# Kernel optimization log

Hardware: AMD Instinct MI355X
Metric: run time of the kernel (lower is better)

## Reference

```python
import jax, jax.numpy as jnp
import numpy as np

HID = 128
N_LAYERS = 6


def _init_linear(key, fan_in, fan_out, scale=None):
    kw, kb = jax.random.split(key)
    s = scale if scale is not None else (1.0 / np.sqrt(fan_in))
    W = jax.random.uniform(kw, (fan_in, fan_out), jnp.float32, -s, s)
    b = jnp.zeros((fan_out,), jnp.float32)
    return W, b


def setup_inputs() -> dict:
    key = jax.random.key(0)
    ks = jax.random.split(key, 16)
    N, E, EC = 50000, 600000, 100000
    x = jax.random.normal(ks[0], (N, 9), jnp.float32)
    edge_index = jax.random.randint(ks[1], (2, E), 0, N, jnp.int64)
    edge_attr = jax.random.normal(ks[2], (E, 11), jnp.float32)
    connectivity = jax.random.randint(ks[3], (EC, 2), 0, N, jnp.int64)
    bc_disp = (jax.random.uniform(ks[4], (N, 1)) < 0.1).astype(jnp.float32)
    prop_I22 = jax.random.uniform(ks[5], (EC,), jnp.float32)

    enc_W1, enc_b1 = _init_linear(ks[6], 9, HID)
    enc_W2, enc_b2 = _init_linear(ks[7], HID, HID)
    # per-layer GN params stacked along axis 0
    msg_in = 2 * HID + 11
    mk = jax.random.split(ks[8], N_LAYERS)
    uk = jax.random.split(ks[9], N_LAYERS)
    mk2 = jax.random.split(ks[10], N_LAYERS)
    msg_W1 = jnp.stack([_init_linear(mk[i], msg_in, HID)[0] for i in range(N_LAYERS)])
    msg_b1 = jnp.zeros((N_LAYERS, HID), jnp.float32)
    msg_W2 = jnp.stack([_init_linear(mk2[i], HID, HID)[0] for i in range(N_LAYERS)])
    msg_b2 = jnp.zeros((N_LAYERS, HID), jnp.float32)
    upd_W = jnp.stack([_init_linear(uk[i], 2 * HID, HID)[0] for i in range(N_LAYERS)])
    upd_b = jnp.zeros((N_LAYERS, HID), jnp.float32)

    ef_W1, ef_b1 = _init_linear(ks[11], 1 + 2 * HID, 64)
    ef_W2, ef_b2 = _init_linear(ks[12], 64, 64)
    ef_W3, ef_b3 = _init_linear(ks[13], 64, 3, scale=0.1 * np.sqrt(6.0 / (64 + 3)))

    return dict(x=x, edge_index=edge_index, edge_attr=edge_attr,
                connectivity=connectivity, bc_disp=bc_disp, prop_I22=prop_I22,
                n_quad_pts=5,
                enc_W1=enc_W1, enc_b1=enc_b1, enc_W2=enc_W2, enc_b2=enc_b2,
                msg_W1=msg_W1, msg_b1=msg_b1, msg_W2=msg_W2, msg_b2=msg_b2,
                upd_W=upd_W, upd_b=upd_b,
                ef_W1=ef_W1, ef_b1=ef_b1, ef_W2=ef_W2, ef_b2=ef_b2,
                ef_W3=ef_W3, ef_b3=ef_b3)


def reference(x, edge_index, edge_attr, connectivity, bc_disp, prop_I22, n_quad_pts,
              enc_W1, enc_b1, enc_W2, enc_b2,
              msg_W1, msg_b1, msg_W2, msg_b2, upd_W, upd_b,
              ef_W1, ef_b1, ef_W2, ef_b2, ef_W3, ef_b3):
    N = x.shape[0]
    silu = jax.nn.silu
    # encoder MLP
    h = silu(x @ enc_W1 + enc_b1)
    h = silu(h @ enc_W2 + enc_b2)
    src, dst = edge_index[0], edge_index[1]
    for l in range(N_LAYERS):
        m_in = jnp.concatenate([h[src], h[dst], edge_attr], axis=-1)  # (E, 2H+11)
        m = silu(m_in @ msg_W1[l] + msg_b1[l]) @ msg_W2[l] + msg_b2[l]
        agg = jax.ops.segment_sum(m, dst, num_segments=N)  # scatter-add
        h = jnp.concatenate([h, agg], axis=-1) @ upd_W[l] + upd_b[l] + h  # residual update
        h = silu(h)
    # continuous edge field evaluation
    n1, n2 = connectivity[:, 0], connectivity[:, 1]
    EC = connectivity.shape[0]
    xi_1d = jnp.linspace(0.0, 1.0, n_quad_pts, dtype=jnp.float32)
    xi = jnp.broadcast_to(xi_1d[None, :, None], (EC, n_quad_pts, 1))
    h_i = jnp.broadcast_to(h[n1][:, None, :], (EC, n_quad_pts, HID))
    h_j = jnp.broadcast_to(h[n2][:, None, :], (EC, n_quad_pts, HID))
    inp = jnp.concatenate([xi, h_i, h_j], axis=-1)  # (EC, n_pts, 1+2H)
    f = silu(inp @ ef_W1 + ef_b1)
    f = silu(f @ ef_W2 + ef_b2)
    fields = f @ ef_W3 + ef_b3  # (EC, n_pts, 3)
    # hard BCs
    bc_mask = bc_disp[:, 0]
    bc_i, bc_j = bc_mask[n1], bc_mask[n2]
    xi_vals = xi[..., 0]
    mask_i = 1.0 - bc_i[:, None] * (1.0 - xi_vals)
    mask_j = 1.0 - bc_j[:, None] * xi_vals
    fields = fields * (mask_i * mask_j)[..., None]
    return h, xi, fields, prop_I22
```

## Files before the change

### kernel.cpp

```cpp
#include <hip/hip_runtime.h>
#include <hip/hip_bf16.h>

#define HID 128
#define EA_DIM 11
#define MSG_IN (2 * HID + EA_DIM)
#define TILE_E 128
#define KCAP 272
#define KB (KCAP * 2)
#define MSG_LDS 139264

typedef __attribute__((ext_vector_type(8))) short short8;
typedef __attribute__((ext_vector_type(16))) float f32x16;
typedef __attribute__((ext_vector_type(4))) float float4v;

__device__ __forceinline__ float siluf(float x) { return x / (1.f + __expf(-x)); }
__device__ __forceinline__ short f2bf(float f) {
    __hip_bfloat16 h = __float2bfloat16(f);
    return *reinterpret_cast<short*>(&h);
}
__device__ __forceinline__ int crow(int r, int khalf) { return (r & 3) + 8 * (r >> 2) + 4 * khalf; }

__global__ __launch_bounds__(128) void encoder_kernel(
    const float* __restrict__ x, const float* __restrict__ W1, const float* __restrict__ b1,
    const float* __restrict__ W2, const float* __restrict__ b2,
    float* __restrict__ h, short* __restrict__ hb)
{
    int i = blockIdx.x, j = threadIdx.x;
    __shared__ float xs[9];
    __shared__ float t1[HID];
    if (j < 9) xs[j] = x[(size_t)i * 9 + j];
    __syncthreads();
    float acc = b1[j];
    #pragma unroll
    for (int k = 0; k < 9; ++k) acc = fmaf(xs[k], W1[k * HID + j], acc);
    t1[j] = siluf(acc);
    __syncthreads();
    float acc2 = b2[j];
    #pragma unroll 8
    for (int k = 0; k < HID; ++k) acc2 = fmaf(t1[k], W2[k * HID + j], acc2);
    float v = siluf(acc2);
    h[(size_t)i * HID + j] = v;
    if (hb) hb[(size_t)i * HID + j] = f2bf(v);
}

__global__ void convert_w_kernel(
    const float* __restrict__ msgW1, const float* __restrict__ msgW2,
    const float* __restrict__ updW,
    const float* __restrict__ efW1, const float* __restrict__ efW2, const float* __restrict__ efW3,
    short* __restrict__ w1t, short* __restrict__ w2t, short* __restrict__ updwt,
    short* __restrict__ efw1t, short* __restrict__ efw2t, short* __restrict__ efw3t, int nl)
{
    int gid = blockIdx.x * blockDim.x + threadIdx.x;
    int n1 = nl * 128 * (KCAP / 8);
    int n2 = nl * 128 * (HID / 8);
    int n3 = nl * 128 * 32;
    int n4 = 64 * 32, n5 = 64 * 8, n6 = 32 * 8;
    short8 v;
    if (gid < n1) {
        int c = gid % (KCAP / 8);
        int rem = gid / (KCAP / 8);
        int n = rem % 128, lay = rem / 128;
        #pragma unroll
        for (int j = 0; j < 8; ++j) {
            int k = c * 8 + j;
            v[j] = (k < MSG_IN) ? f2bf(msgW1[(size_t)lay * MSG_IN * HID + (size_t)k * HID + n]) : (short)0;
        }
        *(short8*)(w1t + ((size_t)lay * 128 + n) * KCAP + c * 8) = v;
    } else if (gid < n1 + n2) {
        int g = gid - n1;
        int c = g % (HID / 8);
        int rem = g / (HID / 8);
        int n = rem % 128, lay = rem / 128;
        #pragma unroll
        for (int j = 0; j < 8; ++j)
            v[j] = f2bf(msgW2[(size_t)lay * HID * HID + (size_t)(c * 8 + j) * HID + n]);
        *(short8*)(w2t + ((size_t)lay * 128 + n) * HID + c * 8) = v;
    } else if (gid < n1 + n2 + n3) {
        int g = gid - n1 - n2;
        int c = g & 31;
        int rem = g >> 5;
        int n = rem & 127, lay = rem >> 7;
        #pragma unroll
        for (int j = 0; j < 8; ++j)
            v[j] = f2bf(updW[(size_t)lay * 256 * 128 + (size_t)(c * 8 + j) * 128 + n]);
        *(short8*)(updwt + ((size_t)lay * 128 + n) * 256 + c * 8) = v;
    } else if (gid < n1 + n2 + n3 + n4) {
        int g = gid - n1 - n2 - n3;
        int c = g & 31, n = g >> 5;
        #pragma unroll
        for (int j = 0; j < 8; ++j)
            v[j] = f2bf(efW1[(size_t)(c * 8 + j + 1) * 64 + n]);
        *(short8*)(efw1t + (size_t)n * 256 + c * 8) = v;
    } else if (gid < n1 + n2 + n3 + n4 + n5) {
        int g = gid - n1 - n2 - n3 - n4;
        int c = g & 7, n = g >> 3;
        #pragma unroll
        for (int j = 0; j < 8; ++j)
            v[j] = f2bf(efW2[(size_t)(c * 8 + j) * 64 + n]);
        *(short8*)(efw2t + (size_t)n * 64 + c * 8) = v;
    } else if (gid < n1 + n2 + n3 + n4 + n5 + n6) {
        int g = gid - n1 - n2 - n3 - n4 - n5;
        int c = g & 7, n = g >> 3;
        #pragma unroll
        for (int j = 0; j < 8; ++j)
            v[j] = (n < 3) ? f2bf(efW3[(size_t)(c * 8 + j) * 3 + n]) : (short)0;
        *(short8*)(efw3t + (size_t)n * 64 + c * 8) = v;
    }
}

__global__ void hist_kernel(const int* __restrict__ ei, int* __restrict__ cnt, int E)
{
    for (int e = blockIdx.x * blockDim.x + threadIdx.x; e < E; e += gridDim.x * blockDim.x)
        atomicAdd(&cnt[ei[(size_t)E + e]], 1);
}
__global__ __launch_bounds__(256) void scanA_kernel(const int* __restrict__ cnt, int* __restrict__ btot, int N)
{
    __shared__ int s[256];
    int i = blockIdx.x * 256 + threadIdx.x;
    s[threadIdx.x] = (i < N) ? cnt[i] : 0;
    __syncthreads();
    for (int o = 128; o > 0; o >>= 1) {
        if (threadIdx.x < o) s[threadIdx.x] += s[threadIdx.x + o];
        __syncthreads();
    }
    if (threadIdx.x == 0) btot[blockIdx.x] = s[0];
}
__global__ __launch_bounds__(1024) void scanB_kernel(int* __restrict__ btot, int nb)
{
    __shared__ int s[1024];
    int t = threadIdx.x;
    int v = (t < nb) ? btot[t] : 0;
    s[t] = v;
    __syncthreads();
    for (int o = 1; o < 1024; o <<= 1) {
        int tv = 0;
        if (t >= o) tv = s[t - o];
        __syncthreads();
        s[t] += tv;
        __syncthreads();
    }
    if (t < nb) btot[t] = s[t] - v;
}
__global__ __launch_bounds__(256) void scanC_kernel(const int* __restrict__ cnt, const int* __restrict__ btot,
                                                    int* __restrict__ cur, int N)
{
    __shared__ int s[256];
    int i = blockIdx.x * 256 + threadIdx.x;
    int t = threadIdx.x;
    int v = (i < N) ? cnt[i] : 0;
    s[t] = v;
    __syncthreads();
    for (int o = 1; o < 256; o <<= 1) {
        int tv = 0;
        if (t >= o) tv = s[t - o];
        __syncthreads();
        s[t] += tv;
        __syncthreads();
    }
    if (i < N) cur[i] = btot[blockIdx.x] + s[t] - v;
}
__global__ void scatter_kernel(const int* __restrict__ ei, int* __restrict__ cur,
                               int* __restrict__ eord, int E)
{
    for (int e = blockIdx.x * blockDim.x + threadIdx.x; e < E; e += gridDim.x * blockDim.x) {
        int d = ei[(size_t)E + e];
        int p = atomicAdd(&cur[d], 1);
        eord[p] = e;
    }
}
__global__ void reorder_kernel(const int* __restrict__ ei, const float* __restrict__ ea,
                               const int* __restrict__ eord,
                               int* __restrict__ srcs_s, int* __restrict__ dsts_s,
                               short* __restrict__ ea_s, int E)
{
    for (int p = blockIdx.x * blockDim.x + threadIdx.x; p < E; p += gridDim.x * blockDim.x) {
        int es = eord[p];
        srcs_s[p] = ei[es];
        dsts_s[p] = ei[(size_t)E + es];
        short tv[16];
        #pragma unroll
        for (int j = 0; j < 16; ++j) tv[j] = 0;
        #pragma unroll
        for (int j = 0; j < EA_DIM; ++j) tv[j] = f2bf(ea[(size_t)es * EA_DIM + j]);
        short8 v0, v1;
        #pragma unroll
        for (int j = 0; j < 8; ++j) { v0[j] = tv[j]; v1[j] = tv[8 + j]; }
        *(short8*)(ea_s + (size_t)p * 16) = v0;
        *(short8*)(ea_s + (size_t)p * 16 + 8) = v1;
    }
}

__global__ __launch_bounds__(512, 1) void msg_mfma_kernel(
    const float* __restrict__ h, const short* __restrict__ hb,
    const int* __restrict__ ei, const float* __restrict__ ea,
    const int* __restrict__ srcs_s, const int* __restrict__ dsts_s, const short* __restrict__ ea_s,
    const short* __restrict__ w1t, const float* __restrict__ b1,
    const short* __restrict__ w2t, const float* __restrict__ b2,
    float* __restrict__ agg, int E, int ntiles)
{
    extern __shared__ char smem[];
    char* sA = smem + 69632;
    __shared__ int dsts[TILE_E];

    int tid = threadIdx.x, ln = tid & 63, wave = tid >> 6;
    int mh = wave & 1, nq4 = wave >> 1;
    int l31 = ln & 31, khalf = ln >> 5;

    {
        int row = tid & 127, grp = tid >> 7;
        for (int c = grp; c < 34; c += 4) {
            short8 v = *(const short8*)(w1t + (size_t)row * KCAP + c * 8);
            *(short8*)(smem + ((row * KB + c * 16) ^ ((row & 7) << 4))) = v;
        }
    }

    int col = nq4 * 32 + l31;
    float b1v = b1[col], b2v = b2[col];
    short8 zer;
    #pragma unroll
    for (int j = 0; j < 8; ++j) zer[j] = 0;
    int ar0 = mh * 64 + l31;
    const short8* w2r = (const short8*)(w2t + (size_t)col * HID);

    bool sorted = (ea_s != nullptr) && (hb != nullptr);

    int pr = tid >> 2, pq = tid & 3;
    int pf_idx = 0; bool pf_valid = false;
    short8 pf_h[8];
    short8 pf_e0 = zer, pf_e1 = zer;

    if (sorted) {
        long ep = (long)blockIdx.x * TILE_E + pr;
        pf_valid = ep < E;
        pf_idx = pf_valid ? ((pq < 2) ? srcs_s[ep] : dsts_s[ep]) : 0;
        const short8* hr8 = (const short8*)(hb + (size_t)pf_idx * HID + (pq & 1) * 64);
        #pragma unroll
        for (int c = 0; c < 8; ++c) pf_h[c] = hr8[c];
        if (pq == 3 && pf_valid) {
            pf_e0 = *(const short8*)(ea_s + (size_t)ep * 16);
            pf_e1 = *(const short8*)(ea_s + (size_t)ep * 16 + 8);
        }
    }

    #pragma unroll 1
    for (int tile = blockIdx.x; tile < ntiles; tile += gridDim.x) {
        __syncthreads();

        if (sorted) {
            int dbase = (pq >> 1) * 256 + (pq & 1) * 128;
            #pragma unroll
            for (int c = 0; c < 8; ++c) {
                short8 v = pf_valid ? pf_h[c] : zer;
                *(short8*)(sA + ((pr * KB + dbase + c * 16) ^ ((pr & 7) << 4))) = v;
            }
            if (pq == 2) dsts[pr] = pf_valid ? pf_idx : -1;
            if (pq == 3) {
                *(short8*)(sA + ((pr * KB + 512) ^ ((pr & 7) << 4))) = pf_valid ? pf_e0 : zer;
                *(short8*)(sA + ((pr * KB + 528) ^ ((pr & 7) << 4))) = pf_valid ? pf_e1 : zer;
            }
        } else {
            int r = pr, q = pq;
            long ep = (long)tile * TILE_E + r;
            bool valid = ep < E;
            int idx = 0;
            if (valid) idx = (q < 2) ? ei[ep] : ei[(size_t)E + ep];
            int half = q & 1;
            int dbase = (q >> 1) * 256 + half * 128;
            if (hb) {
                const short8* hr8 = (const short8*)(hb + (size_t)idx * HID + half * 64);
                #pragma unroll
                for (int c = 0; c < 8; ++c) {
                    short8 v = valid ? hr8[c] : zer;
                    *(short8*)(sA + ((r * KB + dbase + c * 16) ^ ((r & 7) << 4))) = v;
                }
            } else {
                const float* hr = h + (size_t)idx * HID + half * 64;
                #pragma unroll
                for (int c = 0; c < 8; ++c) {
                    short8 v = zer;
                    if (valid) {
                        float4v f0 = *(const float4v*)(hr + c * 8);
                        float4v f1 = *(const float4v*)(hr + c * 8 + 4);
                        #pragma unroll
                        for (int j = 0; j < 4; ++j) { v[j] = f2bf(f0[j]); v[4 + j] = f2bf(f1[j]); }
                    }
                    *(short8*)(sA + ((r * KB + dbase + c * 16) ^ ((r & 7) << 4))) = v;
                }
            }
            if (q == 2) dsts[r] = valid ? idx : -1;
            if (q == 3) {
                short8 v0 = zer, v1 = zer;
                if (valid) {
                    short tv[16];
                    #pragma unroll
                    for (int j = 0; j < 16; ++j) tv[j] = 0;
                    #pragma unroll
                    for (int j = 0; j < EA_DIM; ++j) tv[j] = f2bf(ea[(size_t)ep * EA_DIM + j]);
                    #pragma unroll
                    for (int j = 0; j < 8; ++j) { v0[j] = tv[j]; v1[j] = tv[8 + j]; }
                }
                *(short8*)(sA + ((r * KB + 512) ^ ((r & 7) << 4))) = v0;
                *(short8*)(sA + ((r * KB + 528) ^ ((r & 7) << 4))) = v1;
            }
        }
        __syncthreads();

        if (sorted) {
            long ep = (long)(tile + gridDim.x) * TILE_E + pr;
            pf_valid = ep < E;
            pf_idx = pf_valid ? ((pq < 2) ? srcs_s[ep] : dsts_s[ep]) : 0;
            const short8* hr8 = (const short8*)(hb + (size_t)pf_idx * HID + (pq & 1) * 64);
            #pragma unroll
            for (int c = 0; c < 8; ++c) pf_h[c] = hr8[c];
            if (pq == 3 && pf_valid) {
                pf_e0 = *(const short8*)(ea_s + (size_t)ep * 16);
                pf_e1 = *(const short8*)(ea_s + (size_t)ep * 16 + 8);
            }
        }

        f32x16 acc1[2] = {};
        for (int kk = 0; kk < 17; ++kk) {
            int kb = kk * 32 + khalf * 16;
            short8 a0 = *(short8*)(sA + ((ar0 * KB + kb) ^ ((ar0 & 7) << 4)));
            short8 a1 = *(short8*)(sA + (((ar0 + 32) * KB + kb) ^ (((ar0 + 32) & 7) << 4)));
            short8 w  = *(short8*)(smem + ((col * KB + kb) ^ ((col & 7) << 4)));
            acc1[0] = __builtin_amdgcn_mfma_f32_32x32x16_bf16(a0, w, acc1[0], 0, 0, 0);
            acc1[1] = __builtin_amdgcn_mfma_f32_32x32x16_bf16(a1, w, acc1[1], 0, 0, 0);
        }
        __syncthreads();

        #pragma unroll
        for (int mi = 0; mi < 2; ++mi)
            #pragma unroll
            for (int r = 0; r < 16; ++r) {
                float s = siluf(acc1[mi][r] + b1v);
                int row = mh * 64 + mi * 32 + crow(r, khalf);
                *(short*)(sA + ((row * 256 + col * 2) ^ ((row & 7) << 4))) = f2bf(s);
            }
        __syncthreads();

        f32x16 acc2[2];
        #pragma unroll
        for (int mi = 0; mi < 2; ++mi)
            #pragma unroll
            for (int r = 0; r < 16; ++r) acc2[mi][r] = b2v;
        for (int kk = 0; kk < 8; ++kk) {
            int kb = kk * 32 + khalf * 16;
            short8 a0 = *(short8*)(sA + ((ar0 * 256 + kb) ^ ((ar0 & 7) << 4)));
            short8 a1 = *(short8*)(sA + (((ar0 + 32) * 256 + kb) ^ (((ar0 + 32) & 7) << 4)));
            short8 w  = w2r[kk * 2 + khalf];
            acc2[0] = __builtin_amdgcn_mfma_f32_32x32x16_bf16(a0, w, acc2[0], 0, 0, 0);
            acc2[1] = __builtin_amdgcn_mfma_f32_32x32x16_bf16(a1, w, acc2[1], 0, 0, 0);
        }

        if (sorted) {
            __syncthreads();
            #pragma unroll
            for (int mi = 0; mi < 2; ++mi)
                #pragma unroll
                for (int r = 0; r < 16; ++r) {
                    int row = mh * 64 + mi * 32 + crow(r, khalf);
                    *(float*)(sA + row * 512 + col * 4) = acc2[mi][r];
                }
            __syncthreads();
            {
                int c2 = tid & 63, g = tid >> 6;
                float s0 = 0.f, s1 = 0.f;
                int dprev = -1;
                #pragma unroll 1
                for (int rr = 0; rr < 16; ++rr) {
                    int row = g * 16 + rr;
                    int d = dsts[row];
                    float2 v = *(float2*)(sA + row * 512 + c2 * 8);
                    if (d != dprev) {
                        if (dprev >= 0) {
                            atomicAdd(agg + (size_t)dprev * HID + c2 * 2,     s0);
                            atomicAdd(agg + (size_t)dprev * HID + c2 * 2 + 1, s1);
                        }
                        s0 = 0.f; s1 = 0.f; dprev = d;
                    }
                    if (d >= 0) { s0 += v.x; s1 += v.y; }
                }
                if (dprev >= 0) {
                    atomicAdd(agg + (size_t)dprev * HID + c2 * 2,     s0);
                    atomicAdd(agg + (size_t)dprev * HID + c2 * 2 + 1, s1);
                }
            }
        } else {
            #pragma unroll
            for (int mi = 0; mi < 2; ++mi)
                #pragma unroll
                for (int r = 0; r < 16; ++r) {
                    int row = mh * 64 + mi * 32 + crow(r, khalf);
                    int d = dsts[row];
                    if (d >= 0) atomicAdd(agg + (size_t)d * HID + col, acc2[mi][r]);
                }
        }
    }
}

__global__ __launch_bounds__(256) void upd_mfma_kernel(
    float* __restrict__ h, short* __restrict__ hb, const float* __restrict__ agg,
    const short* __restrict__ updwt, const float* __restrict__ b, int N, int ntiles)
{
    __shared__ char sA[64 * 512];
    int tid = threadIdx.x, ln = tid & 63, wave = tid >> 6;
    int mhalf = wave & 1, nhalf = wave >> 1, l31 = ln & 31, khalf = ln >> 5;
    float bv[2];
    #pragma unroll
    for (int ni = 0; ni < 2; ++ni) bv[ni] = b[nhalf * 64 + ni * 32 + l31];
    short8 zer;
    #pragma unroll
    for (int j = 0; j < 8; ++j) zer[j] = 0;

    #pragma unroll 1
    for (int tile = blockIdx.x; tile < ntiles; tile += gridDim.x) {
        __syncthreads();
        {
            int r = tid >> 2, q = tid & 3;
            int node = tile * 64 + r;
            bool valid = node < N;
            if (q < 2) {
                if (hb) {
                    const short8* hr8 = (const short8*)(hb + (size_t)node * HID + (q & 1) * 64);
                    #pragma unroll
                    for (int c = 0; c < 8; ++c) {
                        short8 v = valid ? hr8[c] : zer;
                        *(short8*)(sA + ((r * 512 + (q & 1) * 128 + c * 16) ^ ((r & 7) << 4))) = v;
                    }
                } else {
                    const float* hr = h + (size_t)node * HID + (q & 1) * 64;
                    #pragma unroll
                    for (int c = 0; c < 8; ++c) {
                        short8 v = zer;
                        if (valid) {
                            float4v f0 = *(const float4v*)(hr + c * 8);
                            float4v f1 = *(const float4v*)(hr + c * 8 + 4);
                            #pragma unroll
                            for (int j = 0; j < 4; ++j) { v[j] = f2bf(f0[j]); v[4 + j] = f2bf(f1[j]); }
                        }
                        *(short8*)(sA + ((r * 512 + (q & 1) * 128 + c * 16) ^ ((r & 7) << 4))) = v;
                    }
                }
            } else {
                const float* ar = agg + (size_t)node * HID + (q & 1) * 64;
                #pragma unroll
                for (int c = 0; c < 8; ++c) {
                    short8 v = zer;
                    if (valid) {
                        float4v f0 = *(const float4v*)(ar + c * 8);
                        float4v f1 = *(const float4v*)(ar + c * 8 + 4);
                        #pragma unroll
                        for (int j = 0; j < 4; ++j) { v[j] = f2bf(f0[j]); v[4 + j] = f2bf(f1[j]); }
                    }
                    *(short8*)(sA + ((r * 512 + 256 + (q & 1) * 128 + c * 16) ^ ((r & 7) << 4))) = v;
                }
            }
        }
        __syncthreads();
        f32x16 acc[2] = {};
        int arow = mhalf * 32 + l31;
        const short* bp0 = updwt + (size_t)(nhalf * 64 + l31) * 256 + khalf * 8;
        const short* bp1 = updwt + (size_t)(nhalf * 64 + 32 + l31) * 256 + khalf * 8;
        for (int kk = 0; kk < 16; ++kk) {
            short8 a  = *(short8*)(sA + ((arow * 512 + kk * 32 + khalf * 16) ^ ((arow & 7) << 4)));
            short8 w0 = *(const short8*)(bp0 + kk * 16);
            short8 w1 = *(const short8*)(bp1 + kk * 16);
            acc[0] = __builtin_amdgcn_mfma_f32_32x32x16_bf16(a, w0, acc[0], 0, 0, 0);
            acc[1] = __builtin_amdgcn_mfma_f32_32x32x16_bf16(a, w1, acc[1], 0, 0, 0);
        }
        #pragma unroll
        for (int ni = 0; ni < 2; ++ni) {
            int col = nhalf * 64 + ni * 32 + l31;
            #pragma unroll
            for (int r = 0; r < 16; ++r) {
                int node = tile * 64 + mhalf * 32 + crow(r, khalf);
                if (node < N) {
                    float val = siluf(acc[ni][r] + bv[ni] + h[(size_t)node * HID + col]);
                    h[(size_t)node * HID + col] = val;
                    if (hb) hb[(size_t)node * HID + col] = f2bf(val);
                }
            }
        }
    }
}

__global__ __launch_bounds__(256) void fields_mfma_kernel(
    const float* __restrict__ h, const short* __restrict__ hb,
    const int* __restrict__ conn, const float* __restrict__ bc,
    const float* __restrict__ efW1, const float* __restrict__ efb1,
    const float* __restrict__ efb2, const float* __restrict__ efb3,
    const short* __restrict__ efw1t, const short* __restrict__ efw2t, const short* __restrict__ efw3t,
    float* __restrict__ f_out, int EC, int nq, int ntiles)
{
    __shared__ char sA1[64 * 512];
    __shared__ char sA2[64 * 128];
    __shared__ char sF2[64 * 128];
    __shared__ float bcis[64], bcjs[64];
    int tid = threadIdx.x, ln = tid & 63, wave = tid >> 6;
    int mhalf = wave & 1, nhalf = wave >> 1, l31 = ln & 31, khalf = ln >> 5;
    int col = nhalf * 32 + l31;
    float w1x = efW1[col];
    float b1v = efb1[col], b2v = efb2[col];
    float b3v = (l31 < 3) ? efb3[l31] : 0.f;
    float inv = (nq > 1) ? 1.f / (float)(nq - 1) : 0.f;
    short8 zer;
    #pragma unroll
    for (int j = 0; j < 8; ++j) zer[j] = 0;

    #pragma unroll 1
    for (int tile = blockIdx.x; tile < ntiles; tile += gridDim.x) {
        __syncthreads();
        {
            int r = tid >> 2, q = tid & 3;
            long p = (long)tile * 64 + r;
            bool valid = p < EC;
            int node = 0;
            if (valid) node = conn[p * 2 + (q >> 1)];
            if (q == 0) {
                bcis[r] = valid ? bc[conn[p * 2]] : 0.f;
                bcjs[r] = valid ? bc[conn[p * 2 + 1]] : 0.f;
            }
            int cbyte = (q >> 1) * 256 + (q & 1) * 128;
            if (hb) {
                const short8* hr8 = (const short8*)(hb + (size_t)node * HID + (q & 1) * 64);
                #pragma unroll
                for (int c = 0; c < 8; ++c) {
                    short8 v = valid ? hr8[c] : zer;
                    *(short8*)(sA1 + ((r * 512 + cbyte + c * 16) ^ ((r & 7) << 4))) = v;
                }
            } else {
                const float* hr = h + (size_t)node * HID + (q & 1) * 64;
                #pragma unroll
                for (int c = 0; c < 8; ++c) {
                    short8 v = zer;
                    if (valid) {
                        float4v f0 = *(const float4v*)(hr + c * 8);
                        float4v f1 = *(const float4v*)(hr + c * 8 + 4);
                        #pragma unroll
                        for (int j = 0; j < 4; ++j) { v[j] = f2bf(f0[j]); v[4 + j] = f2bf(f1[j]); }
                    }
                    *(short8*)(sA1 + ((r * 512 + cbyte + c * 16) ^ ((r & 7) << 4))) = v;
                }
            }
        }
        __syncthreads();
        f32x16 hp = {};
        int arow = mhalf * 32 + l31;
        for (int kk = 0; kk < 16; ++kk) {
            short8 a = *(short8*)(sA1 + ((arow * 512 + kk * 32 + khalf * 16) ^ ((arow & 7) << 4)));
            short8 b = *(const short8*)(efw1t + (size_t)col * 256 + kk * 16 + khalf * 8);
            hp = __builtin_amdgcn_mfma_f32_32x32x16_bf16(a, b, hp, 0, 0, 0);
        }
        #pragma unroll
        for (int r = 0; r < 16; ++r) hp[r] += b1v;

        for (int q = 0; q < nq; ++q) {
            float xi = (float)q * inv;
            #pragma unroll
            for (int r = 0; r < 16; ++r) {
                float f1 = siluf(fmaf(xi, w1x, hp[r]));
                int row = mhalf * 32 + crow(r, khalf);
                *(short*)(sA2 + ((row * 128 + col * 2) ^ ((row & 7) << 4))) = f2bf(f1);
            }
            __syncthreads();
            f32x16 f2a = {};
            for (int kk = 0; kk < 4; ++kk) {
                short8 a = *(short8*)(sA2 + ((arow * 128 + kk * 32 + khalf * 16) ^ ((l31 & 7) << 4)));
                short8 b = *(const short8*)(efw2t + (size_t)col * 64 + kk * 16 + khalf * 8);
                f2a = __builtin_amdgcn_mfma_f32_32x32x16_bf16(a, b, f2a, 0, 0, 0);
            }
            #pragma unroll
            for (int r = 0; r < 16; ++r) {
                float f2 = siluf(f2a[r] + b2v);
                int row = mhalf * 32 + crow(r, khalf);
                *(short*)(sF2 + ((row * 128 + col * 2) ^ ((row & 7) << 4))) = f2bf(f2);
            }
            __syncthreads();
            f32x16 oa = {};
            for (int kk = 0; kk < 4; ++kk) {
                short8 a = *(short8*)(sF2 + ((arow * 128 + kk * 32 + khalf * 16) ^ ((l31 & 7) << 4)));
                short8 b = *(const short8*)(efw3t + (size_t)l31 * 64 + kk * 16 + khalf * 8);
                oa = __builtin_amdgcn_mfma_f32_32x32x16_bf16(a, b, oa, 0, 0, 0);
            }
            if (nhalf == 0 && l31 < 3) {
                #pragma unroll
                for (int r = 0; r < 16; ++r) {
                    int row = mhalf * 32 + crow(r, khalf);
                    long p = (long)tile * 64 + row;
                    if (p < EC) {
                        float mask = (1.f - bcis[row] * (1.f - xi)) * (1.f - bcjs[row] * xi);
                        f_out[((size_t)p * nq + q) * 3 + l31] = (oa[r] + b3v) * mask;
                    }
                }
            }
        }
    }
}

__global__ void aux_kernel(const float* __restrict__ prop, float* __restrict__ out_p,
                           float* __restrict__ out_xi, int EC, int nq, float inv)
{
    int i = blockIdx.x * blockDim.x + threadIdx.x;
    if (i < EC) out_p[i] = prop[i];
    if (i < EC * nq) out_xi[i] = (float)(i % nq) * inv;
}

extern "C" void kernel_launch(void* const* d_in, const int* in_sizes, int n_in,
                              void* d_out, int out_size, void* d_ws, size_t ws_size,
                              hipStream_t stream) {
    const float* x     = (const float*)d_in[0];
    const int*   ei    = (const int*)d_in[1];
    const float* ea    = (const float*)d_in[2];
    const int*   conn  = (const int*)d_in[3];
    const float* bc    = (const float*)d_in[4];
    const float* prop  = (const float*)d_in[5];
    const float* encW1 = (const float*)d_in[7];
    const float* encb1 = (const float*)d_in[8];
    const float* encW2 = (const float*)d_in[9];
    const float* encb2 = (const float*)d_in[10];
    const float* msgW1 = (const float*)d_in[11];
    const float* msgb1 = (const float*)d_in[12];
    const float* msgW2 = (const float*)d_in[13];
    const float* msgb2 = (const float*)d_in[14];
    const float* updW  = (const float*)d_in[15];
    const float* updb  = (const float*)d_in[16];
    const float* efW1  = (const float*)d_in[17];
    const float* efb1  = (const float*)d_in[18];
    const float* efW2  = (const float*)d_in[19];
    const float* efb2  = (const float*)d_in[20];
    const float* efW3  = (const float*)d_in[21];
    const float* efb3  = (const float*)d_in[22];

    int N  = in_sizes[0] / 9;
    int E  = in_sizes[1] / 2;
    int EC = in_sizes[5];
    int nl = in_sizes[11] / (MSG_IN * HID);
    int nq = (int)(((long long)out_size - (long long)N * HID - EC) / (4LL * EC));

    float* out    = (float*)d_out;
    float* h      = out;
    float* out_xi = out + (size_t)N * HID;
    float* out_f  = out_xi + (size_t)EC * nq;
    float* out_p  = out_f + (size_t)EC * nq * 3;

    size_t w1t_e = (size_t)nl * 128 * KCAP;
    size_t w2t_e = (size_t)nl * 128 * HID;
    size_t updwt_e = (size_t)nl * 128 * 256;
    size_t efw1t_e = 64 * 256, efw2t_e = 64 * 64, efw3t_e = 32 * 64;
    short* w1t   = (short*)d_ws;
    short* w2t   = w1t + w1t_e;
    short* updwt = w2t + w2t_e;
    short* efw1t = updwt + updwt_e;
    short* efw2t = efw1t + efw1t_e;
    short* efw3t = efw2t + efw2t_e;
    size_t wbytes = (w1t_e + w2t_e + updwt_e + efw1t_e + efw2t_e + efw3t_e) * 2;
    wbytes = (wbytes + 255) & ~(size_t)255;
    size_t hb_bytes  = (size_t)N * HID * 2;
    size_t agg_bytes = (size_t)N * HID * 4;
    size_t sort_bytes = ((size_t)2 * N + 1024 + (size_t)3 * E) * 4 + (size_t)E * 32;

    short* hb = nullptr;
    float* agg;
    int *icnt = nullptr, *icur = nullptr, *btot = nullptr, *eord = nullptr;
    int *srcs_s = nullptr, *dsts_s = nullptr;
    short* ea_s = nullptr;
    if (ws_size >= wbytes + hb_bytes + agg_bytes + sort_bytes) {
        char* p = (char*)d_ws + wbytes;
        hb = (short*)p;      p += hb_bytes;
        agg = (float*)p;     p += agg_bytes;
        icnt = (int*)p;      p += (size_t)N * 4;
        icur = (int*)p;      p += (size_t)N * 4;
        btot = (int*)p;      p += 1024 * 4;
        eord = (int*)p;      p += (size_t)E * 4;
        srcs_s = (int*)p;    p += (size_t)E * 4;
        dsts_s = (int*)p;    p += (size_t)E * 4;
        ea_s = (short*)p;
    } else if (ws_size >= wbytes + hb_bytes + agg_bytes) {
        hb  = (short*)((char*)d_ws + wbytes);
        agg = (float*)((char*)d_ws + wbytes + hb_bytes);
    } else {
        agg = (float*)((char*)d_ws + wbytes);
    }

    hipFuncSetAttribute((const void*)msg_mfma_kernel,
                        hipFuncAttributeMaxDynamicSharedMemorySize, MSG_LDS);

    encoder_kernel<<<N, 128, 0, stream>>>(x, encW1, encb1, encW2, encb2, h, hb);

    {
        int chunks = nl * 128 * (KCAP / 8) + nl * 128 * (HID / 8) + nl * 128 * 32
                   + 64 * 32 + 64 * 8 + 32 * 8;
        convert_w_kernel<<<(chunks + 255) / 256, 256, 0, stream>>>(
            msgW1, msgW2, updW, efW1, efW2, efW3,
            w1t, w2t, updwt, efw1t, efw2t, efw3t, nl);
    }

    if (ea_s) {
        int nb = (N + 255) / 256;
        hipMemsetAsync(icnt, 0, (size_t)N * 4, stream);
        hist_kernel<<<512, 256, 0, stream>>>(ei, icnt, E);
        scanA_kernel<<<nb, 256, 0, stream>>>(icnt, btot, N);
        scanB_kernel<<<1, 1024, 0, stream>>>(btot, nb);
        scanC_kernel<<<nb, 256, 0, stream>>>(icnt, btot, icur, N);
        scatter_kernel<<<512, 256, 0, stream>>>(ei, icur, eord, E);
        reorder_kernel<<<512, 256, 0, stream>>>(ei, ea, eord, srcs_s, dsts_s, ea_s, E);
    }

    int ntiles = (E + TILE_E - 1) / TILE_E;
    int utiles = (N + 63) / 64;
    for (int l = 0; l < nl; ++l) {
        hipMemsetAsync(agg, 0, agg_bytes, stream);
        msg_mfma_kernel<<<256, 512, MSG_LDS, stream>>>(
            h, hb, ei, ea, srcs_s, dsts_s, ea_s,
            w1t + (size_t)l * 128 * KCAP, msgb1 + (size_t)l * HID,
            w2t + (size_t)l * 128 * HID,  msgb2 + (size_t)l * HID,
            agg, E, ntiles);
        upd_mfma_kernel<<<512, 256, 0, stream>>>(
            h, hb, agg, updwt + (size_t)l * 128 * 256, updb + (size_t)l * HID, N, utiles);
    }

    int ftiles = (EC + 63) / 64;
    fields_mfma_kernel<<<512, 256, 0, stream>>>(
        h, hb, conn, bc, efW1, efb1, efb2, efb3, efw1t, efw2t, efw3t,
        out_f, EC, nq, ftiles);

    float inv = (nq > 1) ? 1.f / (float)(nq - 1) : 0.f;
    aux_kernel<<<(EC * nq + 255) / 256, 256, 0, stream>>>(prop, out_p, out_xi, EC, nq, inv);
}
```

Baseline: 1.760 ms.

## Hold W1 fragments in registers and shrink LDS for two blocks per CU

The message MLP kernel no longer stages the first-layer weight matrix in shared memory. Each lane keeps its 17 W1 fragments in registers, which cuts LDS to about 100KB, and the launch bound is raised to allow two 512-thread blocks per CU. The LDS regions are re-laid out so the second-layer activations and the fp32 output staging use separate buffers, which removes two barriers, and the swizzle is now computed from the address bits. Holding W1 in registers raises VGPR pressure and may cause spills or limit the hoped-for occupancy gain, and the buffer aliasing changes need careful correctness checks.

```diff
diff --git a/kernel.cpp b/kernel.cpp
--- a/kernel.cpp
+++ b/kernel.cpp
@@ -7,7 +7,7 @@
 #define TILE_E 128
 #define KCAP 272
 #define KB (KCAP * 2)
-#define MSG_LDS 139264
+#define MSG_LDS 102400
 
 typedef __attribute__((ext_vector_type(8))) short short8;
 typedef __attribute__((ext_vector_type(16))) float f32x16;
@@ -19,6 +19,14 @@
     return *reinterpret_cast<short*>(&h);
 }
 __device__ __forceinline__ int crow(int r, int khalf) { return (r & 3) + 8 * (r >> 2) + 4 * khalf; }
+
+__device__ __forceinline__ int swa1(int row, int off) {
+    int a = row * KB + off;
+    return a ^ (((a >> 7) & 7) << 4);
+}
+__device__ __forceinline__ int swa2(int row, int off) {
+    return (row * 256 + off) ^ ((row & 7) << 4);
+}
 
 __global__ __launch_bounds__(128) void encoder_kernel(
     const float* __restrict__ x, const float* __restrict__ W1, const float* __restrict__ b1,
@@ -190,7 +198,7 @@
     }
 }
 
-__global__ __launch_bounds__(512, 1) void msg_mfma_kernel(
+__global__ __launch_bounds__(512, 2) void msg_mfma_kernel(
     const float* __restrict__ h, const short* __restrict__ hb,
     const int* __restrict__ ei, const float* __restrict__ ea,
     const int* __restrict__ srcs_s, const int* __restrict__ dsts_s, const short* __restrict__ ea_s,
@@ -199,20 +207,12 @@
     float* __restrict__ agg, int E, int ntiles)
 {
     extern __shared__ char smem[];
-    char* sA = smem + 69632;
+    char* sA2r = smem + 69632;
     __shared__ int dsts[TILE_E];
 
     int tid = threadIdx.x, ln = tid & 63, wave = tid >> 6;
     int mh = wave & 1, nq4 = wave >> 1;
     int l31 = ln & 31, khalf = ln >> 5;
-
-    {
-        int row = tid & 127, grp = tid >> 7;
-        for (int c = grp; c < 34; c += 4) {
-            short8 v = *(const short8*)(w1t + (size_t)row * KCAP + c * 8);
-            *(short8*)(smem + ((row * KB + c * 16) ^ ((row & 7) << 4))) = v;
-        }
-    }
 
     int col = nq4 * 32 + l31;
     float b1v = b1[col], b2v = b2[col];
@@ -222,6 +222,13 @@
     int ar0 = mh * 64 + l31;
     const short8* w2r = (const short8*)(w2t + (size_t)col * HID);
 
+    short8 w1f[17];
+    {
+        const short8* w1r = (const short8*)(w1t + (size_t)col * KCAP);
+        #pragma unroll
+        for (int kk = 0; kk < 17; ++kk) w1f[kk] = w1r[kk * 2 + khalf];
+    }
+
     bool sorted = (ea_s != nullptr) && (hb != nullptr);
 
     int pr = tid >> 2, pq = tid & 3;
@@ -251,12 +258,12 @@
             #pragma unroll
             for (int c = 0; c < 8; ++c) {
                 short8 v = pf_valid ? pf_h[c] : zer;
-                *(short8*)(sA + ((pr * KB + dbase + c * 16) ^ ((pr & 7) << 4))) = v;
+                *(short8*)(smem + swa1(pr, dbase + c * 16)) = v;
             }
             if (pq == 2) dsts[pr] = pf_valid ? pf_idx : -1;
             if (pq == 3) {
-                *(short8*)(sA + ((pr * KB + 512) ^ ((pr & 7) << 4))) = pf_valid ? pf_e0 : zer;
-                *(short8*)(sA + ((pr * KB + 528) ^ ((pr & 7) << 4))) = pf_valid ? pf_e1 : zer;
+                *(short8*)(smem + swa1(pr, 512)) = pf_valid ? pf_e0 : zer;
+                *(short8*)(smem + swa1(pr, 528)) = pf_valid ? pf_e1 : zer;
             }
         } else {
             int r = pr, q = pq;
@@ -271,7 +278,7 @@
                 #pragma unroll
                 for (int c = 0; c < 8; ++c) {
                     short8 v = valid ? hr8[c] : zer;
-                    *(short8*)(sA + ((r * KB + dbase + c * 16) ^ ((r & 7) << 4))) = v;
+                    *(short8*)(smem + swa1(r, dbase + c * 16)) = v;
                 }
             } else {
                 const float* hr = h + (size_t)idx * HID + half * 64;
@@ -284,7 +291,7 @@
                         #pragma unroll
                         for (int j = 0; j < 4; ++j) { v[j] = f2bf(f0[j]); v[4 + j] = f2bf(f1[j]); }
                     }
-                    *(short8*)(sA + ((r * KB + dbase + c * 16) ^ ((r & 7) << 4))) = v;
+                    *(short8*)(smem + swa1(r, dbase + c * 16)) = v;
                 }
             }
             if (q == 2) dsts[r] = valid ? idx : -1;
@@ -299,8 +306,8 @@
                     #pragma unroll
                     for (int j = 0; j < 8; ++j) { v0[j] = tv[j]; v1[j] = tv[8 + j]; }
                 }
-                *(short8*)(sA + ((r * KB + 512) ^ ((r & 7) << 4))) = v0;
-                *(short8*)(sA + ((r * KB + 528) ^ ((r & 7) << 4))) = v1;
+                *(short8*)(smem + swa1(r, 512)) = v0;
+                *(short8*)(smem + swa1(r, 528)) = v1;
             }
         }
         __syncthreads();
@@ -319,15 +326,14 @@
         }
 
         f32x16 acc1[2] = {};
+        #pragma unroll
         for (int kk = 0; kk < 17; ++kk) {
             int kb = kk * 32 + khalf * 16;
-            short8 a0 = *(short8*)(sA + ((ar0 * KB + kb) ^ ((ar0 & 7) << 4)));
-            short8 a1 = *(short8*)(sA + (((ar0 + 32) * KB + kb) ^ (((ar0 + 32) & 7) << 4)));
-            short8 w  = *(short8*)(smem + ((col * KB + kb) ^ ((col & 7) << 4)));
-            acc1[0] = __builtin_amdgcn_mfma_f32_32x32x16_bf16(a0, w, acc1[0], 0, 0, 0);
-            acc1[1] = __builtin_amdgcn_mfma_f32_32x32x16_bf16(a1, w, acc1[1], 0, 0, 0);
-        }
-        __syncthreads();
+            short8 a0 = *(short8*)(smem + swa1(ar0, kb));
+            short8 a1 = *(short8*)(smem + swa1(ar0 + 32, kb));
+            acc1[0] = __builtin_amdgcn_mfma_f32_32x32x16_bf16(a0, w1f[kk], acc1[0], 0, 0, 0);
+            acc1[1] = __builtin_amdgcn_mfma_f32_32x32x16_bf16(a1, w1f[kk], acc1[1], 0, 0, 0);
+        }
 
         #pragma unroll
         for (int mi = 0; mi < 2; ++mi)
@@ -335,7 +341,7 @@
             for (int r = 0; r < 16; ++r) {
                 float s = siluf(acc1[mi][r] + b1v);
                 int row = mh * 64 + mi * 32 + crow(r, khalf);
-                *(short*)(sA + ((row * 256 + col * 2) ^ ((row & 7) << 4))) = f2bf(s);
+                *(short*)(sA2r + swa2(row, col * 2)) = f2bf(s);
             }
         __syncthreads();
 
@@ -344,23 +350,23 @@
         for (int mi = 0; mi < 2; ++mi)
             #pragma unroll
             for (int r = 0; r < 16; ++r) acc2[mi][r] = b2v;
+        #pragma unroll
         for (int kk = 0; kk < 8; ++kk) {
             int kb = kk * 32 + khalf * 16;
-            short8 a0 = *(short8*)(sA + ((ar0 * 256 + kb) ^ ((ar0 & 7) << 4)));
-            short8 a1 = *(short8*)(sA + (((ar0 + 32) * 256 + kb) ^ (((ar0 + 32) & 7) << 4)));
+            short8 a0 = *(short8*)(sA2r + swa2(ar0, kb));
+            short8 a1 = *(short8*)(sA2r + swa2(ar0 + 32, kb));
             short8 w  = w2r[kk * 2 + khalf];
             acc2[0] = __builtin_amdgcn_mfma_f32_32x32x16_bf16(a0, w, acc2[0], 0, 0, 0);
             acc2[1] = __builtin_amdgcn_mfma_f32_32x32x16_bf16(a1, w, acc2[1], 0, 0, 0);
         }
 
         if (sorted) {
-            __syncthreads();
             #pragma unroll
             for (int mi = 0; mi < 2; ++mi)
                 #pragma unroll
                 for (int r = 0; r < 16; ++r) {
                     int row = mh * 64 + mi * 32 + crow(r, khalf);
-                    *(float*)(sA + row * 512 + col * 4) = acc2[mi][r];
+                    *(float*)(smem + row * 512 + col * 4) = acc2[mi][r];
                 }
             __syncthreads();
             {
@@ -371,7 +377,7 @@
                 for (int rr = 0; rr < 16; ++rr) {
                     int row = g * 16 + rr;
                     int d = dsts[row];
-                    float2 v = *(float2*)(sA + row * 512 + c2 * 8);
+                    float2 v = *(float2*)(smem + row * 512 + c2 * 8);
                     if (d != dprev) {
                         if (dprev >= 0) {
                             atomicAdd(agg + (size_t)dprev * HID + c2 * 2,     s0);
```

Result: slower. 2.928 ms (+66.3%).
